# Performance work log

Measured on AMD Instinct MI355X. Metric: run time of the kernel, lower is better.

## Reference

```python
import jax, jax.numpy as jnp
import numpy as np


def setup_inputs() -> dict:
    B, N, D, M = 512, 128, 768, 32  # bags, num_class, embed_dim, max bag size
    rng = np.random.default_rng(0)
    sizes = rng.integers(8, 25, size=B)  # variable bag sizes in [8, 24], all <= M
    offsets = np.concatenate([[0], np.cumsum(sizes)]).astype(np.int32)
    nsum = int(offsets[-1])
    scope = np.stack([offsets[:-1], offsets[1:]], axis=1)  # (B, 2) [start, end)

    key = jax.random.key(0)
    k1, k2, k3 = jax.random.split(key, 3)
    rep = jax.random.normal(k1, (nsum, D), dtype=jnp.float32)
    fc_weight = jax.random.normal(k2, (N, D), dtype=jnp.float32) * 0.02
    fc_bias = jax.random.normal(k3, (N,), dtype=jnp.float32) * 0.02
    return {
        "rep": rep,
        "fc_weight": fc_weight,
        "fc_bias": fc_bias,
        "scope": jnp.asarray(scope),
        "max_bag": M,
    }


def reference(rep, fc_weight, fc_bias, scope, max_bag):
    """IntraBagAttention forward (train=False, bag_size=0 branch), ragged bags
    rewritten as padded/masked dense ops.

    rep:       (nsum, D) sentence-encoder outputs
    fc_weight: (N, D), fc_bias: (N,)
    scope:     (B, 2) int [start, end) per bag; max_bag: static int pad bound
    returns:   (B, N) per-relation bag scores
    """
    nsum = rep.shape[0]
    starts = scope[:, 0]
    sizes = scope[:, 1] - scope[:, 0]
    pos = jnp.arange(max_bag)
    idx = jnp.clip(starts[:, None] + pos[None, :], 0, nsum - 1)  # (B, M)
    valid = pos[None, :] < sizes[:, None]                        # (B, M)
    bag = rep[idx]                                               # (B, M, D)

    # att_score = rep @ fc.weight.data.T ; .data => no grad through this use
    w_att = jax.lax.stop_gradient(fc_weight)
    att = jnp.einsum('bmd,nd->bnm', bag, w_att)                  # (B, N, M)
    att = jnp.where(valid[:, None, :], att, -jnp.inf)
    sm = jax.nn.softmax(att, axis=-1)                            # per-bag softmax over sentences

    # weighted segment sum: one attended rep per relation per bag
    rfer = jnp.einsum('bnm,bmd->bnd', sm, bag)                   # (B, N, D)

    # fc(rep_for_each_rel) -> (B, N, N); softmax over classes; take diagonal
    full = jnp.einsum('bnd,kd->bnk', rfer, fc_weight) + fc_bias  # (B, N, N)
    probs = jax.nn.softmax(full, axis=-1)
    return jnp.diagonal(probs, axis1=1, axis2=2)                 # (B, N)
```

## Files before the change

### kernel.cpp

```cpp
#include <hip/hip_runtime.h>
#include <math.h>

#define B_BAGS 512
#define N_REL  128
#define D_DIM  768

typedef __attribute__((ext_vector_type(8))) short  bf16x8;
typedef __attribute__((ext_vector_type(4))) float  f32x4;

__device__ inline unsigned pack_hi(float f0, float f1) {
    return __builtin_amdgcn_perm(__float_as_uint(f1), __float_as_uint(f0), 0x07060302u);
}
__device__ inline float trunc_res(float f) {
    return f - __uint_as_float(__float_as_uint(f) & 0xFFFF0000u);
}

__global__ void afrag_prep(const float* __restrict__ rep,
                           unsigned* __restrict__ Afrag, int nsum) {
    const int grp = blockIdx.x;
    const int t   = threadIdx.x;
    #pragma unroll
    for (int i = 0; i < 24; ++i) {
        const int u   = i * 256 + t;
        const int gs  = u >> 8;
        const int rem = u & 255;
        const int r   = rem >> 4;
        const int jw  = rem & 15;
        int row = grp * 16 + r;
        row = (row > nsum - 1) ? (nsum - 1) : row;
        const float2 f = *(const float2*)&rep[(size_t)row * D_DIM + gs * 32 + jw * 2];
        const unsigned base = (unsigned)((grp * 24 + gs) * 2) * 256 + rem;
        Afrag[base]       = pack_hi(f.x, f.y);
        Afrag[base + 256] = pack_hi(trunc_res(f.x), trunc_res(f.y));
    }
}

__global__ void build_bfrag(const float* __restrict__ W, unsigned* __restrict__ Bfrag) {
    int flat = blockIdx.x * 256 + threadIdx.x;
    int lane = flat & 63;
    int tile = (flat >> 6) & 7;
    int s    = flat >> 9;
    int n  = tile * 16 + (lane & 15);
    int k0 = s * 32 + (lane >> 4) * 8;
    const float* src = &W[n * D_DIM + k0];
    float f[8];
    #pragma unroll
    for (int j = 0; j < 8; ++j) f[j] = src[j];
    unsigned hi[4], lo[4];
    #pragma unroll
    for (int q = 0; q < 4; ++q) {
        hi[q] = pack_hi(f[2*q], f[2*q+1]);
        lo[q] = pack_hi(trunc_res(f[2*q]), trunc_res(f[2*q+1]));
    }
    unsigned base = (unsigned)(((s * 8 + tile) * 2) * 64 + lane) * 4;
    *(uint4*)&Bfrag[base]          = make_uint4(hi[0], hi[1], hi[2], hi[3]);
    *(uint4*)&Bfrag[base + 64 * 4] = make_uint4(lo[0], lo[1], lo[2], lo[3]);
}

__global__ __launch_bounds__(512, 4) void bag_fused(
    const unsigned* __restrict__ Afrag,
    const unsigned* __restrict__ Bfrag,
    const float*    __restrict__ bias,
    const int*      __restrict__ scope,
    float*          __restrict__ out,
    int nsum)
{
    __shared__ f32x4    Gpart[2][2][8][64];
    __shared__ unsigned Gfrag[8 * 2 * 64 * 4];
    __shared__ unsigned SMfrag[8 * 2 * 64 * 4];

    const int t = threadIdx.x;
    const int b = blockIdx.x;
    const int start = scope[2 * b];
    const int size  = scope[2 * b + 1] - start;

    const int wv   = t >> 6;
    const int lane = t & 63;
    const int nl15 = lane & 15;
    const int lg   = lane >> 4;
    const int h    = wv >> 2;
    const int q    = wv & 3;

    unsigned abase[2][2];
    #pragma unroll
    for (int mt = 0; mt < 2; ++mt) {
        int row = start + mt * 16 + nl15;
        row = (row > nsum - 1) ? (nsum - 1) : row;
        const unsigned grp = (unsigned)row >> 4;
        const unsigned r   = (unsigned)row & 15;
        #pragma unroll
        for (int p = 0; p < 2; ++p)
            abase[mt][p] = ((grp * 24 + h * 12) * 2 + p) * 256 + r * 16 + lg * 4;
    }
    unsigned bbase[2][2];
    #pragma unroll
    for (int ntl = 0; ntl < 2; ++ntl)
        #pragma unroll
        for (int p = 0; p < 2; ++p)
            bbase[ntl][p] = (((h * 12) * 8 + q * 2 + ntl) * 2 + p) * 256 + lane * 4;

    f32x4 acc[2][2][2];
    #pragma unroll
    for (int mt = 0; mt < 2; ++mt)
        #pragma unroll
        for (int ntl = 0; ntl < 2; ++ntl) {
            acc[mt][ntl][0] = f32x4{0.f, 0.f, 0.f, 0.f};
            acc[mt][ntl][1] = f32x4{0.f, 0.f, 0.f, 0.f};
        }

    #pragma unroll
    for (int s = 0; s < 12; ++s) {
        bf16x8 ah[2], al[2], bh[2], bl[2];
        #pragma unroll
        for (int mt = 0; mt < 2; ++mt) {
            ah[mt] = *(const bf16x8*)&Afrag[abase[mt][0] + s * 512];
            al[mt] = *(const bf16x8*)&Afrag[abase[mt][1] + s * 512];
        }
        #pragma unroll
        for (int ntl = 0; ntl < 2; ++ntl) {
            bh[ntl] = *(const bf16x8*)&Bfrag[bbase[ntl][0] + s * 4096];
            bl[ntl] = *(const bf16x8*)&Bfrag[bbase[ntl][1] + s * 4096];
        }
        #pragma unroll
        for (int ntl = 0; ntl < 2; ++ntl)
            #pragma unroll
            for (int mt = 0; mt < 2; ++mt) {
                acc[mt][ntl][0] = __builtin_amdgcn_mfma_f32_16x16x32_bf16(ah[mt], bh[ntl], acc[mt][ntl][0], 0, 0, 0);
                acc[mt][ntl][1] = __builtin_amdgcn_mfma_f32_16x16x32_bf16(ah[mt], bl[ntl], acc[mt][ntl][1], 0, 0, 0);
                acc[mt][ntl][1] = __builtin_amdgcn_mfma_f32_16x16x32_bf16(al[mt], bh[ntl], acc[mt][ntl][1], 0, 0, 0);
            }
    }

    #pragma unroll
    for (int mt = 0; mt < 2; ++mt)
        #pragma unroll
        for (int ntl = 0; ntl < 2; ++ntl)
            Gpart[h][mt][q * 2 + ntl][lane] = acc[mt][ntl][0] + acc[mt][ntl][1];
    __syncthreads();

    const int T = wv;
    float gv[2][4], smv[2][4];
    #pragma unroll
    for (int mt = 0; mt < 2; ++mt) {
        const f32x4 p0 = Gpart[0][mt][T][lane];
        const f32x4 p1 = Gpart[1][mt][T][lane];
        #pragma unroll
        for (int r = 0; r < 4; ++r) gv[mt][r] = p0[r] + p1[r];
    }

    float vmax = -INFINITY;
    #pragma unroll
    for (int mt = 0; mt < 2; ++mt)
        #pragma unroll
        for (int r = 0; r < 4; ++r) {
            const int m = mt * 16 + lg * 4 + r;
            if (m < size) vmax = fmaxf(vmax, gv[mt][r]);
        }
    vmax = fmaxf(vmax, __shfl_xor(vmax, 16));
    vmax = fmaxf(vmax, __shfl_xor(vmax, 32));

    float ssum = 0.f;
    #pragma unroll
    for (int mt = 0; mt < 2; ++mt)
        #pragma unroll
        for (int r = 0; r < 4; ++r) {
            const int m = mt * 16 + lg * 4 + r;
            float e = (m < size) ? __expf(gv[mt][r] - vmax) : 0.f;
            smv[mt][r] = e;
            ssum += e;
        }
    ssum += __shfl_xor(ssum, 16);
    ssum += __shfl_xor(ssum, 32);
    const float inv = 1.f / ssum;
    #pragma unroll
    for (int mt = 0; mt < 2; ++mt)
        #pragma unroll
        for (int r = 0; r < 4; ++r) smv[mt][r] *= inv;

    #pragma unroll
    for (int mt = 0; mt < 2; ++mt)
        #pragma unroll
        for (int rp = 0; rp < 4; rp += 2) {
            const int m     = mt * 16 + lg * 4 + rp;
            const int lane2 = (m >> 3) * 16 + nl15;
            const int word  = (m >> 1) & 3;
            const int ihi = ((T * 2 + 0) * 64 + lane2) * 4 + word;
            const int ilo = ((T * 2 + 1) * 64 + lane2) * 4 + word;
            Gfrag[ihi]  = pack_hi(gv[mt][rp], gv[mt][rp + 1]);
            Gfrag[ilo]  = pack_hi(trunc_res(gv[mt][rp]), trunc_res(gv[mt][rp + 1]));
            SMfrag[ihi] = pack_hi(smv[mt][rp], smv[mt][rp + 1]);
            SMfrag[ilo] = pack_hi(trunc_res(smv[mt][rp]), trunc_res(smv[mt][rp + 1]));
        }
    __syncthreads();

    float bias_r[8];
    #pragma unroll
    for (int ct = 0; ct < 8; ++ct) bias_r[ct] = bias[ct * 16 + nl15];

    f32x4 facc[8];
    #pragma unroll
    for (int ct = 0; ct < 8; ++ct) facc[ct] = f32x4{0.f, 0.f, 0.f, 0.f};

    const bf16x8 ah2 = *(const bf16x8*)&SMfrag[((T * 2 + 0) * 64 + lane) * 4];
    const bf16x8 al2 = *(const bf16x8*)&SMfrag[((T * 2 + 1) * 64 + lane) * 4];
    #pragma unroll
    for (int ct = 0; ct < 8; ++ct) {
        const bf16x8 bh = *(const bf16x8*)&Gfrag[((ct * 2 + 0) * 64 + lane) * 4];
        const bf16x8 bl = *(const bf16x8*)&Gfrag[((ct * 2 + 1) * 64 + lane) * 4];
        facc[ct] = __builtin_amdgcn_mfma_f32_16x16x32_bf16(ah2, bh, facc[ct], 0, 0, 0);
        facc[ct] = __builtin_amdgcn_mfma_f32_16x16x32_bf16(ah2, bl, facc[ct], 0, 0, 0);
        facc[ct] = __builtin_amdgcn_mfma_f32_16x16x32_bf16(al2, bh, facc[ct], 0, 0, 0);
    }

    #pragma unroll
    for (int r = 0; r < 4; ++r) {
        float s[8];
        #pragma unroll
        for (int ct = 0; ct < 8; ++ct) s[ct] = facc[ct][r] + bias_r[ct];

        float mx = s[0];
        #pragma unroll
        for (int ct = 1; ct < 8; ++ct) mx = fmaxf(mx, s[ct]);
        mx = fmaxf(mx, __shfl_xor(mx, 1));
        mx = fmaxf(mx, __shfl_xor(mx, 2));
        mx = fmaxf(mx, __shfl_xor(mx, 4));
        mx = fmaxf(mx, __shfl_xor(mx, 8));

        float l = 0.f;
        #pragma unroll
        for (int ct = 0; ct < 8; ++ct) l += __expf(s[ct] - mx);
        l += __shfl_xor(l, 1);
        l += __shfl_xor(l, 2);
        l += __shfl_xor(l, 4);
        l += __shfl_xor(l, 8);

        const int nl = lg * 4 + r;
        float sd = s[0];
        #pragma unroll
        for (int ct = 1; ct < 8; ++ct) sd = (ct == T) ? s[ct] : sd;
        if (nl15 == nl) {
            out[b * N_REL + T * 16 + nl] = __expf(sd - mx) / l;
        }
    }
}

extern "C" void kernel_launch(void* const* d_in, const int* in_sizes, int n_in,
                              void* d_out, int out_size, void* d_ws, size_t ws_size,
                              hipStream_t stream) {
    const float* rep   = (const float*)d_in[0];
    const float* W     = (const float*)d_in[1];
    const float* bias  = (const float*)d_in[2];
    const int*   scope = (const int*)d_in[3];

    const int nsum   = in_sizes[0] / D_DIM;
    const int groups = (nsum + 15) >> 4;

    unsigned* Bfrag = (unsigned*)d_ws;
    unsigned* Afrag = (unsigned*)((char*)d_ws + 393216);

    build_bfrag<<<48, 256, 0, stream>>>(W, Bfrag);
    afrag_prep<<<groups, 256, 0, stream>>>(rep, Afrag, nsum);
    bag_fused<<<B_BAGS, 512, 0, stream>>>(Afrag, Bfrag, bias, scope,
                                          (float*)d_out, nsum);
}
```

Baseline: 103.3 us.

## Compute attention logits as one dense split-K GEMM over all rows

Removes the separate A-fragment prep kernel and the per-bag attention GEMM. A new kernel tiles all sentence rows in 128-row strips and splits D into four chunks. It converts rep to hi/lo bf16 in shared memory and writes partial rep·W^T logits to a workspace. The bag kernel then sums the four partials per row instead of recomputing the GEMM for padded 32-row windows, which cuts redundant MFMA work on overlapping and padded rows. In exchange it adds a global round trip for the partial logit buffer and launch bounds drop to 2 blocks.

```diff
diff --git a/kernel.cpp b/kernel.cpp
--- a/kernel.cpp
+++ b/kernel.cpp
@@ -4,6 +4,7 @@
 #define B_BAGS 512
 #define N_REL  128
 #define D_DIM  768
+#define NCHUNK 4
 
 typedef __attribute__((ext_vector_type(8))) short  bf16x8;
 typedef __attribute__((ext_vector_type(4))) float  f32x4;
@@ -13,26 +14,6 @@
 }
 __device__ inline float trunc_res(float f) {
     return f - __uint_as_float(__float_as_uint(f) & 0xFFFF0000u);
-}
-
-__global__ void afrag_prep(const float* __restrict__ rep,
-                           unsigned* __restrict__ Afrag, int nsum) {
-    const int grp = blockIdx.x;
-    const int t   = threadIdx.x;
-    #pragma unroll
-    for (int i = 0; i < 24; ++i) {
-        const int u   = i * 256 + t;
-        const int gs  = u >> 8;
-        const int rem = u & 255;
-        const int r   = rem >> 4;
-        const int jw  = rem & 15;
-        int row = grp * 16 + r;
-        row = (row > nsum - 1) ? (nsum - 1) : row;
-        const float2 f = *(const float2*)&rep[(size_t)row * D_DIM + gs * 32 + jw * 2];
-        const unsigned base = (unsigned)((grp * 24 + gs) * 2) * 256 + rem;
-        Afrag[base]       = pack_hi(f.x, f.y);
-        Afrag[base + 256] = pack_hi(trunc_res(f.x), trunc_res(f.y));
-    }
 }
 
 __global__ void build_bfrag(const float* __restrict__ W, unsigned* __restrict__ Bfrag) {
@@ -57,15 +38,118 @@
     *(uint4*)&Bfrag[base + 64 * 4] = make_uint4(lo[0], lo[1], lo[2], lo[3]);
 }
 
-__global__ __launch_bounds__(512, 4) void bag_fused(
-    const unsigned* __restrict__ Afrag,
+__global__ __launch_bounds__(512, 2) void h_gemm(
+    const float*    __restrict__ rep,
     const unsigned* __restrict__ Bfrag,
-    const float*    __restrict__ bias,
-    const int*      __restrict__ scope,
-    float*          __restrict__ out,
+    float*          __restrict__ Hp,
+    int nsum, int hstride)
+{
+    __shared__ unsigned As[2 * 128 * 36];
+
+    const int t     = threadIdx.x;
+    const int strip = blockIdx.x;
+    const int chunk = blockIdx.y;
+
+    const int wv   = t >> 6;
+    const int lane = t & 63;
+    const int nl15 = lane & 15;
+    const int lg   = lane >> 4;
+    const int j    = wv & 3;
+    const int nh   = wv >> 2;
+
+    const int srow = t >> 2;
+    const int scq  = t & 3;
+    int grow = strip * 128 + srow;
+    grow = (grow > nsum - 1) ? (nsum - 1) : grow;
+    const float* srp = &rep[(size_t)grow * D_DIM + chunk * 192 + scq * 16];
+
+    f32x4 acc[2][4][2];
+    #pragma unroll
+    for (int mt = 0; mt < 2; ++mt)
+        #pragma unroll
+        for (int i = 0; i < 4; ++i) {
+            acc[mt][i][0] = f32x4{0.f, 0.f, 0.f, 0.f};
+            acc[mt][i][1] = f32x4{0.f, 0.f, 0.f, 0.f};
+        }
+
+    unsigned afo[2][2];
+    #pragma unroll
+    for (int mt = 0; mt < 2; ++mt) {
+        const int row = (j * 2 + mt) * 16 + nl15;
+        afo[mt][0] = (0 * 128 + row) * 36 + lg * 4;
+        afo[mt][1] = (1 * 128 + row) * 36 + lg * 4;
+    }
+
+    #pragma unroll
+    for (int st = 0; st < 3; ++st) {
+        if (st) __syncthreads();
+        {
+            const float4 v0 = *(const float4*)&srp[st * 64];
+            const float4 v1 = *(const float4*)&srp[st * 64 + 4];
+            const float4 v2 = *(const float4*)&srp[st * 64 + 8];
+            const float4 v3 = *(const float4*)&srp[st * 64 + 12];
+            unsigned hi[8], lo[8];
+            const float f[16] = {v0.x,v0.y,v0.z,v0.w, v1.x,v1.y,v1.z,v1.w,
+                                 v2.x,v2.y,v2.z,v2.w, v3.x,v3.y,v3.z,v3.w};
+            #pragma unroll
+            for (int w = 0; w < 8; ++w) {
+                hi[w] = pack_hi(f[2*w], f[2*w+1]);
+                lo[w] = pack_hi(trunc_res(f[2*w]), trunc_res(f[2*w+1]));
+            }
+            const unsigned bh = (0 * 128 + srow) * 36 + scq * 8;
+            const unsigned bl = (1 * 128 + srow) * 36 + scq * 8;
+            *(uint4*)&As[bh]     = make_uint4(hi[0], hi[1], hi[2], hi[3]);
+            *(uint4*)&As[bh + 4] = make_uint4(hi[4], hi[5], hi[6], hi[7]);
+            *(uint4*)&As[bl]     = make_uint4(lo[0], lo[1], lo[2], lo[3]);
+            *(uint4*)&As[bl + 4] = make_uint4(lo[4], lo[5], lo[6], lo[7]);
+        }
+        __syncthreads();
+
+        #pragma unroll
+        for (int g = 0; g < 2; ++g) {
+            const int gsg = chunk * 6 + st * 2 + g;
+            bf16x8 ah[2], al[2];
+            #pragma unroll
+            for (int mt = 0; mt < 2; ++mt) {
+                ah[mt] = *(const bf16x8*)&As[afo[mt][0] + g * 16];
+                al[mt] = *(const bf16x8*)&As[afo[mt][1] + g * 16];
+            }
+            #pragma unroll
+            for (int i = 0; i < 4; ++i) {
+                const int nt = nh * 4 + i;
+                const bf16x8 bh = *(const bf16x8*)&Bfrag[((gsg * 8 + nt) * 2 + 0) * 256 + lane * 4];
+                const bf16x8 bl = *(const bf16x8*)&Bfrag[((gsg * 8 + nt) * 2 + 1) * 256 + lane * 4];
+                #pragma unroll
+                for (int mt = 0; mt < 2; ++mt) {
+                    acc[mt][i][0] = __builtin_amdgcn_mfma_f32_16x16x32_bf16(ah[mt], bh, acc[mt][i][0], 0, 0, 0);
+                    acc[mt][i][1] = __builtin_amdgcn_mfma_f32_16x16x32_bf16(ah[mt], bl, acc[mt][i][1], 0, 0, 0);
+                    acc[mt][i][1] = __builtin_amdgcn_mfma_f32_16x16x32_bf16(al[mt], bh, acc[mt][i][1], 0, 0, 0);
+                }
+            }
+        }
+    }
+
+    float* H = Hp + (size_t)chunk * hstride;
+    #pragma unroll
+    for (int mt = 0; mt < 2; ++mt) {
+        const int rowb = strip * 128 + (j * 2 + mt) * 16 + lg * 4;
+        #pragma unroll
+        for (int i = 0; i < 4; ++i) {
+            const int col = (nh * 4 + i) * 16 + nl15;
+            #pragma unroll
+            for (int r = 0; r < 4; ++r)
+                H[(size_t)(rowb + r) * N_REL + col] = acc[mt][i][0][r] + acc[mt][i][1][r];
+        }
+    }
+}
+
+__global__ __launch_bounds__(512, 2) void bag_out(
+    const float* __restrict__ Hp, int hstride,
+    const float* __restrict__ bias,
+    const int*   __restrict__ scope,
+    float*       __restrict__ out,
     int nsum)
 {
-    __shared__ f32x4    Gpart[2][2][8][64];
     __shared__ unsigned Gfrag[8 * 2 * 64 * 4];
     __shared__ unsigned SMfrag[8 * 2 * 64 * 4];
 
@@ -78,75 +162,19 @@
     const int lane = t & 63;
     const int nl15 = lane & 15;
     const int lg   = lane >> 4;
-    const int h    = wv >> 2;
-    const int q    = wv & 3;
-
-    unsigned abase[2][2];
-    #pragma unroll
-    for (int mt = 0; mt < 2; ++mt) {
-        int row = start + mt * 16 + nl15;
-        row = (row > nsum - 1) ? (nsum - 1) : row;
-        const unsigned grp = (unsigned)row >> 4;
-        const unsigned r   = (unsigned)row & 15;
-        #pragma unroll
-        for (int p = 0; p < 2; ++p)
-            abase[mt][p] = ((grp * 24 + h * 12) * 2 + p) * 256 + r * 16 + lg * 4;
-    }
-    unsigned bbase[2][2];
-    #pragma unroll
-    for (int ntl = 0; ntl < 2; ++ntl)
-        #pragma unroll
-        for (int p = 0; p < 2; ++p)
-            bbase[ntl][p] = (((h * 12) * 8 + q * 2 + ntl) * 2 + p) * 256 + lane * 4;
-
-    f32x4 acc[2][2][2];
-    #pragma unroll
-    for (int mt = 0; mt < 2; ++mt)
-        #pragma unroll
-        for (int ntl = 0; ntl < 2; ++ntl) {
-            acc[mt][ntl][0] = f32x4{0.f, 0.f, 0.f, 0.f};
-            acc[mt][ntl][1] = f32x4{0.f, 0.f, 0.f, 0.f};
-        }
-
-    #pragma unroll
-    for (int s = 0; s < 12; ++s) {
-        bf16x8 ah[2], al[2], bh[2], bl[2];
-        #pragma unroll
-        for (int mt = 0; mt < 2; ++mt) {
-            ah[mt] = *(const bf16x8*)&Afrag[abase[mt][0] + s * 512];
-            al[mt] = *(const bf16x8*)&Afrag[abase[mt][1] + s * 512];
-        }
-        #pragma unroll
-        for (int ntl = 0; ntl < 2; ++ntl) {
-            bh[ntl] = *(const bf16x8*)&Bfrag[bbase[ntl][0] + s * 4096];
-            bl[ntl] = *(const bf16x8*)&Bfrag[bbase[ntl][1] + s * 4096];
-        }
-        #pragma unroll
-        for (int ntl = 0; ntl < 2; ++ntl)
-            #pragma unroll
-            for (int mt = 0; mt < 2; ++mt) {
-                acc[mt][ntl][0] = __builtin_amdgcn_mfma_f32_16x16x32_bf16(ah[mt], bh[ntl], acc[mt][ntl][0], 0, 0, 0);
-                acc[mt][ntl][1] = __builtin_amdgcn_mfma_f32_16x16x32_bf16(ah[mt], bl[ntl], acc[mt][ntl][1], 0, 0, 0);
-                acc[mt][ntl][1] = __builtin_amdgcn_mfma_f32_16x16x32_bf16(al[mt], bh[ntl], acc[mt][ntl][1], 0, 0, 0);
-            }
-    }
-
-    #pragma unroll
-    for (int mt = 0; mt < 2; ++mt)
-        #pragma unroll
-        for (int ntl = 0; ntl < 2; ++ntl)
-            Gpart[h][mt][q * 2 + ntl][lane] = acc[mt][ntl][0] + acc[mt][ntl][1];
-    __syncthreads();
-
-    const int T = wv;
+    const int T    = wv;
+
     float gv[2][4], smv[2][4];
     #pragma unroll
-    for (int mt = 0; mt < 2; ++mt) {
-        const f32x4 p0 = Gpart[0][mt][T][lane];
-        const f32x4 p1 = Gpart[1][mt][T][lane];
-        #pragma unroll
-        for (int r = 0; r < 4; ++r) gv[mt][r] = p0[r] + p1[r];
-    }
+    for (int mt = 0; mt < 2; ++mt)
+        #pragma unroll
+        for (int r = 0; r < 4; ++r) {
+            int row = start + mt * 16 + lg * 4 + r;
+            row = (row > nsum - 1) ? (nsum - 1) : row;
+            const float* p = &Hp[(size_t)row * N_REL + T * 16 + nl15];
+            gv[mt][r] = p[0] + p[(size_t)hstride] + p[(size_t)hstride * 2]
+                             + p[(size_t)hstride * 3];
+        }
 
     float vmax = -INFINITY;
     #pragma unroll
@@ -252,14 +280,15 @@
     const float* bias  = (const float*)d_in[2];
     const int*   scope = (const int*)d_in[3];
 
-    const int nsum   = in_sizes[0] / D_DIM;
-    const int groups = (nsum + 15) >> 4;
+    const int nsum    = in_sizes[0] / D_DIM;
+    const int strips  = (nsum + 127) >> 7;
+    const int hstride = strips * 128 * N_REL;
 
     unsigned* Bfrag = (unsigned*)d_ws;
-    unsigned* Afrag = (unsigned*)((char*)d_ws + 393216);
+    float*    Hp    = (float*)((char*)d_ws + 393216);
 
     build_bfrag<<<48, 256, 0, stream>>>(W, Bfrag);
-    afrag_prep<<<groups, 256, 0, stream>>>(rep, Afrag, nsum);
-    bag_fused<<<B_BAGS, 512, 0, stream>>>(Afrag, Bfrag, bias, scope,
-                                          (float*)d_out, nsum);
-}
+    h_gemm<<<dim3(strips, NCHUNK), 512, 0, stream>>>(rep, Bfrag, Hp, nsum, hstride);
+    bag_out<<<B_BAGS, 512, 0, stream>>>(Hp, hstride, bias, scope,
+                                        (float*)d_out, nsum);
+}
```

Measured after the change: 100.9 us. 2.3% less time.
